# Optimization experiments

Hardware: AMD Instinct MI355X
Metric: run time of the kernel (lower is better)

The kernel has to match this reference:

```python
import jax, jax.numpy as jnp
import numpy as np

N_QUBITS = 8
N_Q_LAYERS = 4
TARGET = 0
B, N, H = 64, 512, 512


def _apply_1q(state, U, w):
    # apply 2x2 complex gate U on wire w of state with shape (2,)*n
    state = jnp.tensordot(U, state, axes=((1,), (w,)))
    return jnp.moveaxis(state, 0, w)


def _cnot(state, c, t):
    s0 = jnp.take(state, 0, axis=c)
    s1 = jnp.take(state, 1, axis=c)
    t_ = t - 1 if t > c else t
    s1 = jnp.flip(s1, axis=t_)  # X on target where control=1
    return jnp.stack([s0, s1], axis=c)


def _ry(theta):
    c, s = jnp.cos(theta / 2), jnp.sin(theta / 2)
    return jnp.stack([jnp.stack([c, -s]), jnp.stack([s, c])]).astype(jnp.complex64)


def _rx(theta):
    c, s = jnp.cos(theta / 2), jnp.sin(theta / 2)
    z = jnp.zeros_like(c)
    re = jnp.stack([jnp.stack([c, z]), jnp.stack([z, c])])
    im = jnp.stack([jnp.stack([z, s]), jnp.stack([s, z])])
    return (re.astype(jnp.complex64) - 1j * im.astype(jnp.complex64))


def _circuit(angles, weights):
    # AngleEmbedding(rotation='Y') + BasicEntanglerLayers(RX + CNOT ring) + <Z_i>
    n = N_QUBITS
    state = jnp.zeros((2,) * n, dtype=jnp.complex64).at[(0,) * n].set(1.0)
    for w in range(n):
        state = _apply_1q(state, _ry(angles[w]), w)
    for l in range(N_Q_LAYERS):
        for w in range(n):
            state = _apply_1q(state, _rx(weights[l, w]), w)
        for w in range(n):
            state = _cnot(state, w, (w + 1) % n)
    probs = state.real ** 2 + state.imag ** 2
    zs = []
    for i in range(n):
        p = probs.sum(axis=tuple(a for a in range(n) if a != i))  # [2]
        zs.append(p[0] - p[1])
    return jnp.stack(zs)  # [n_qubits]


def setup_inputs() -> dict:
    key = jax.random.key(0)
    ks = jax.random.split(key, 10)
    adj = jax.random.uniform(ks[1], (N, N), dtype=jnp.float32)
    norm_adj = adj / adj.sum(axis=1, keepdims=True)  # row-normalized adjacency
    sH = 1.0 / np.sqrt(H)
    return {
        "x": jax.random.normal(ks[0], (B, N, H), dtype=jnp.float32),
        "norm_adj": norm_adj,
        "W_gcn_w": jax.random.normal(ks[2], (H, H), dtype=jnp.float32) * sH,
        "W_gcn_b": jax.random.normal(ks[3], (H,), dtype=jnp.float32) * sH,
        "pre_w": jax.random.normal(ks[4], (N_QUBITS, H), dtype=jnp.float32) * sH,
        "pre_b": jax.random.normal(ks[5], (N_QUBITS,), dtype=jnp.float32) * sH,
        "post_w": jax.random.normal(ks[6], (H, N_QUBITS), dtype=jnp.float32) * (1.0 / np.sqrt(N_QUBITS)),
        "post_b": jax.random.normal(ks[7], (H,), dtype=jnp.float32) * (1.0 / np.sqrt(N_QUBITS)),
        "q_weights": jax.random.uniform(ks[8], (N_Q_LAYERS, N_QUBITS), dtype=jnp.float32) * 2.0 * jnp.pi,
    }


def reference(x, norm_adj, W_gcn_w, W_gcn_b, pre_w, pre_b, post_w, post_b, q_weights):
    # classical GCN aggregation over all N nodes
    x_agg = jnp.einsum('ij,bjh->bih', norm_adj, x)  # [B,N,H]
    x_agg = jax.nn.gelu(x_agg @ W_gcn_w.T + W_gcn_b, approximate=False)
    # dropout is identity in eval mode
    tgt = x_agg[:, TARGET, :]  # [B,H]
    x_qin = jnp.tanh(tgt @ pre_w.T + pre_b) * jnp.pi  # [B,n_qubits]
    q_out = jax.vmap(lambda a: _circuit(a, q_weights))(x_qin)  # [B,n_qubits]
    q_out = q_out @ post_w.T + post_b  # [B,H]
    out = x_agg.at[:, TARGET, :].set(q_out)
    return out
```

## Files before the change

### kernel.cpp

```cpp
#include <hip/hip_runtime.h>
#include <hip/hip_bf16.h>
#include <math.h>

#define B_  64
#define D_  512
#define NQ  8
#define NL  4

typedef __bf16 bf16;
typedef float  f32x4  __attribute__((ext_vector_type(4)));
typedef bf16   bf16x8 __attribute__((ext_vector_type(8)));

__device__ __forceinline__ void async_load16(const bf16* g, bf16* l) {
    __builtin_amdgcn_global_load_lds(
        (const __attribute__((address_space(1))) void*)g,
        (__attribute__((address_space(3))) void*)l, 16, 0, 0);
}

__global__ __launch_bounds__(256) void convert_kernel(const float* __restrict__ src,
                                                      bf16* __restrict__ dst, int n8) {
    int i = blockIdx.x * 256 + threadIdx.x;
    if (i < n8) {
        const float4 v0 = *(const float4*)(src + (size_t)i * 8);
        const float4 v1 = *(const float4*)(src + (size_t)i * 8 + 4);
        bf16x8 p;
        p[0] = (bf16)v0.x; p[1] = (bf16)v0.y; p[2] = (bf16)v0.z; p[3] = (bf16)v0.w;
        p[4] = (bf16)v1.x; p[5] = (bf16)v1.y; p[6] = (bf16)v1.z; p[7] = (bf16)v1.w;
        *(bf16x8*)(dst + (size_t)i * 8) = p;
    }
}

__global__ __launch_bounds__(256) void convert2_kernel(const float* __restrict__ s0,
                                                       const float* __restrict__ s1,
                                                       bf16* __restrict__ dst, int n8each) {
    int i = blockIdx.x * 256 + threadIdx.x;
    if (i < 2 * n8each) {
        const float* s = (i < n8each) ? (s0 + (size_t)i * 8)
                                      : (s1 + (size_t)(i - n8each) * 8);
        const float4 v0 = *(const float4*)s;
        const float4 v1 = *(const float4*)(s + 4);
        bf16x8 p;
        p[0] = (bf16)v0.x; p[1] = (bf16)v0.y; p[2] = (bf16)v0.z; p[3] = (bf16)v0.w;
        p[4] = (bf16)v1.x; p[5] = (bf16)v1.y; p[6] = (bf16)v1.z; p[7] = (bf16)v1.w;
        *(bf16x8*)(dst + (size_t)i * 8) = p;
    }
}

template <int GELU>
__global__ __launch_bounds__(256) void gemm_nt_dma(const bf16* __restrict__ A,
                                                   const bf16* __restrict__ Bv,
                                                   const float* __restrict__ bias,
                                                   void* __restrict__ Cout) {
    __shared__ bf16 As[2][128 * 64];
    __shared__ bf16 Bs[2][128 * 64];

    const int flat = blockIdx.y * 16 + blockIdx.x;
    const int xcd  = flat & 7;
    const int idx  = flat >> 3;
    const int b    = (xcd << 3) | (idx >> 4);
    const int tile = idx & 15;
    const int m0   = (tile >> 2) * 128;
    const int n0   = (tile & 3) * 128;

    const int t    = threadIdx.x;
    const int lane = t & 63;
    const int w    = t >> 6;
    const int wr   = (w >> 1) * 64;
    const int wc   = (w & 1) * 64;
    const int l15  = lane & 15;
    const int quad = lane >> 4;

    f32x4 acc[4][4];
    for (int i = 0; i < 4; i++)
        for (int j = 0; j < 4; j++) acc[i][j] = (f32x4)(0.0f);

    const bf16* Bb = Bv + (size_t)b * D_ * D_;

    const int rl = lane >> 3;
    const int ck = (lane & 7) ^ rl;

    #pragma unroll
    for (int j = 0; j < 4; j++) {
        const int rbase = w * 32 + j * 8;
        async_load16(A  + (size_t)(m0 + rbase + rl) * D_ + ck * 8, &As[0][rbase * 64]);
        async_load16(Bb + (size_t)(n0 + rbase + rl) * D_ + ck * 8, &Bs[0][rbase * 64]);
    }
    __syncthreads();

    #pragma unroll
    for (int s = 0; s < 8; s++) {
        const int p = s & 1;
        if (s < 7) {
            const int k0 = (s + 1) * 64;
            #pragma unroll
            for (int j = 0; j < 4; j++) {
                const int rbase = w * 32 + j * 8;
                async_load16(A  + (size_t)(m0 + rbase + rl) * D_ + k0 + ck * 8,
                             &As[p ^ 1][rbase * 64]);
                async_load16(Bb + (size_t)(n0 + rbase + rl) * D_ + k0 + ck * 8,
                             &Bs[p ^ 1][rbase * 64]);
            }
        }
        #pragma unroll
        for (int kk = 0; kk < 2; kk++) {
            bf16x8 af[4], bfr[4];
            #pragma unroll
            for (int mt = 0; mt < 4; mt++) {
                const int row = wr + mt * 16 + l15;
                const int sl  = (kk * 4 + quad) ^ (l15 & 7);
                af[mt] = *(const bf16x8*)&As[p][row * 64 + sl * 8];
            }
            #pragma unroll
            for (int nt = 0; nt < 4; nt++) {
                const int row = wc + nt * 16 + l15;
                const int sl  = (kk * 4 + quad) ^ (l15 & 7);
                bfr[nt] = *(const bf16x8*)&Bs[p][row * 64 + sl * 8];
            }
            #pragma unroll
            for (int mt = 0; mt < 4; mt++)
                #pragma unroll
                for (int nt = 0; nt < 4; nt++)
                    acc[mt][nt] = __builtin_amdgcn_mfma_f32_16x16x32_bf16(af[mt], bfr[nt], acc[mt][nt], 0, 0, 0);
        }
        __syncthreads();
    }

    if (GELU == 0) {
        bf16* Cb = (bf16*)Cout + (size_t)b * D_ * D_;
        for (int mt = 0; mt < 4; mt++) {
            int row = m0 + wr + mt * 16 + quad * 4;
            for (int nt = 0; nt < 4; nt++) {
                int col = n0 + wc + nt * 16 + l15;
                for (int r = 0; r < 4; r++)
                    Cb[(size_t)(row + r) * D_ + col] = (bf16)acc[mt][nt][r];
            }
        }
    } else {
        float* Cb = (float*)Cout + (size_t)b * D_ * D_;
        for (int mt = 0; mt < 4; mt++) {
            int row = m0 + wr + mt * 16 + quad * 4;
            for (int nt = 0; nt < 4; nt++) {
                int col = n0 + wc + nt * 16 + l15;
                float bv = bias[col];
                for (int r = 0; r < 4; r++) {
                    float v = acc[mt][nt][r] + bv;
                    Cb[(size_t)(row + r) * D_ + col] = 0.5f * v * (1.0f + erff(v * 0.70710678118654752f));
                }
            }
        }
    }
}

#define PITCH 40
template <int GELU>
__global__ __launch_bounds__(256) void gemm_nt_legacy(const float* __restrict__ A,
                                                      const bf16* __restrict__ Bv,
                                                      const float* __restrict__ bias,
                                                      void* __restrict__ Cout) {
    __shared__ bf16 As[128 * PITCH];
    __shared__ bf16 Bs[128 * 32];
    const int b    = blockIdx.y;
    const int tile = blockIdx.x;
    const int m0   = (tile >> 2) * 128;
    const int n0   = (tile & 3) * 128;
    const int t    = threadIdx.x;
    const int lane = t & 63;
    const int w    = t >> 6;
    const int wr   = (w >> 1) * 64;
    const int wc   = (w & 1) * 64;
    const int l15  = lane & 15;
    const int quad = lane >> 4;

    f32x4 acc[4][4];
    for (int i = 0; i < 4; i++)
        for (int j = 0; j < 4; j++) acc[i][j] = (f32x4)(0.0f);

    const bf16* Bb = Bv + (size_t)b * D_ * D_;

    for (int k0 = 0; k0 < D_; k0 += 32) {
        for (int c = t; c < 512; c += 256) {
            int row = c >> 2, ch = c & 3;
            const float* s = A + (size_t)(m0 + row) * D_ + k0 + ch * 8;
            const float4 v0 = *(const float4*)s;
            const float4 v1 = *(const float4*)(s + 4);
            bf16x8 p;
            p[0] = (bf16)v0.x; p[1] = (bf16)v0.y; p[2] = (bf16)v0.z; p[3] = (bf16)v0.w;
            p[4] = (bf16)v1.x; p[5] = (bf16)v1.y; p[6] = (bf16)v1.z; p[7] = (bf16)v1.w;
            *(bf16x8*)&As[row * PITCH + ch * 8] = p;
        }
        {
            int rl = lane >> 2;
            int kchunk = (lane & 3) ^ ((lane >> 3) & 3);
            #pragma unroll
            for (int j = 0; j < 2; j++) {
                int rbase = w * 32 + j * 16;
                async_load16(Bb + (size_t)(n0 + rbase + rl) * D_ + k0 + kchunk * 8, &Bs[rbase * 32]);
            }
        }
        __syncthreads();
        bf16x8 af[4], bfr[4];
        #pragma unroll
        for (int mt = 0; mt < 4; mt++)
            af[mt] = *(const bf16x8*)&As[(wr + mt * 16 + l15) * PITCH + quad * 8];
        #pragma unroll
        for (int nt = 0; nt < 4; nt++) {
            int row = wc + nt * 16 + l15;
            int kx  = quad ^ ((l15 >> 1) & 3);
            bfr[nt] = *(const bf16x8*)&Bs[row * 32 + kx * 8];
        }
        #pragma unroll
        for (int mt = 0; mt < 4; mt++)
            #pragma unroll
            for (int nt = 0; nt < 4; nt++)
                acc[mt][nt] = __builtin_amdgcn_mfma_f32_16x16x32_bf16(af[mt], bfr[nt], acc[mt][nt], 0, 0, 0);
        __syncthreads();
    }

    if (GELU == 0) {
        bf16* Cb = (bf16*)Cout + (size_t)b * D_ * D_;
        for (int mt = 0; mt < 4; mt++) {
            int row = m0 + wr + mt * 16 + quad * 4;
            for (int nt = 0; nt < 4; nt++) {
                int col = n0 + wc + nt * 16 + l15;
                for (int r = 0; r < 4; r++)
                    Cb[(size_t)(row + r) * D_ + col] = (bf16)acc[mt][nt][r];
            }
        }
    } else {
        float* Cb = (float*)Cout + (size_t)b * D_ * D_;
        for (int mt = 0; mt < 4; mt++) {
            int row = m0 + wr + mt * 16 + quad * 4;
            for (int nt = 0; nt < 4; nt++) {
                int col = n0 + wc + nt * 16 + l15;
                float bv = bias[col];
                for (int r = 0; r < 4; r++) {
                    float v = acc[mt][nt][r] + bv;
                    Cb[(size_t)(row + r) * D_ + col] = 0.5f * v * (1.0f + erff(v * 0.70710678118654752f));
                }
            }
        }
    }
}

__global__ __launch_bounds__(64) void quantum_kernel(float* __restrict__ out,
                                                     const float* __restrict__ pre_w,
                                                     const float* __restrict__ pre_b,
                                                     const float* __restrict__ post_w,
                                                     const float* __restrict__ post_b,
                                                     const float* __restrict__ qw) {
    const int b = blockIdx.x;
    const int l = threadIdx.x;
    float* row0 = out + (size_t)b * D_ * D_;

    float tg[8];
    #pragma unroll
    for (int j = 0; j < 8; j++) tg[j] = row0[l + 64 * j];

    float ang[NQ];
    #pragma unroll
    for (int q = 0; q < NQ; q++) {
        float s = 0.f;
        #pragma unroll
        for (int j = 0; j < 8; j++) s += tg[j] * pre_w[q * D_ + l + 64 * j];
        #pragma unroll
        for (int m = 32; m >= 1; m >>= 1) s += __shfl_xor(s, m, 64);
        ang[q] = tanhf(s + pre_b[q]) * 3.14159265358979323846f;
    }

    float cw[NQ], sw[NQ];
    #pragma unroll
    for (int w = 0; w < NQ; w++) { cw[w] = cosf(0.5f * ang[w]); sw[w] = sinf(0.5f * ang[w]); }
    float re[4], im[4];
    #pragma unroll
    for (int r = 0; r < 4; r++) {
        int idx = l * 4 + r;
        float a = 1.f;
        #pragma unroll
        for (int w = 0; w < NQ; w++) a *= ((idx >> (7 - w)) & 1) ? sw[w] : cw[w];
        re[r] = a; im[r] = 0.f;
    }

    for (int lay = 0; lay < NL; lay++) {
        #pragma unroll
        for (int w = 0; w < 6; w++) {
            float th = 0.5f * qw[lay * NQ + w];
            float c = cosf(th), s = sinf(th);
            int m = 1 << (5 - w);
            #pragma unroll
            for (int r = 0; r < 4; r++) {
                float pre_ = __shfl_xor(re[r], m, 64);
                float pim_ = __shfl_xor(im[r], m, 64);
                re[r] = c * re[r] + s * pim_;
                im[r] = c * im[r] - s * pre_;
            }
        }
        {
            float th = 0.5f * qw[lay * NQ + 6];
            float c = cosf(th), s = sinf(th);
            float or0 = re[0], or1 = re[1], or2 = re[2], or3 = re[3];
            float oi0 = im[0], oi1 = im[1], oi2 = im[2], oi3 = im[3];
            re[0] = c * or0 + s * oi2;  im[0] = c * oi0 - s * or2;
            re[1] = c * or1 + s * oi3;  im[1] = c * oi1 - s * or3;
            re[2] = c * or2 + s * oi0;  im[2] = c * oi2 - s * or0;
            re[3] = c * or3 + s * oi1;  im[3] = c * oi3 - s * or1;
        }
        {
            float th = 0.5f * qw[lay * NQ + 7];
            float c = cosf(th), s = sinf(th);
            float or0 = re[0], or1 = re[1], or2 = re[2], or3 = re[3];
            float oi0 = im[0], oi1 = im[1], oi2 = im[2], oi3 = im[3];
            re[0] = c * or0 + s * oi1;  im[0] = c * oi0 - s * or1;
            re[1] = c * or1 + s * oi0;  im[1] = c * oi1 - s * or0;
            re[2] = c * or2 + s * oi3;  im[2] = c * oi2 - s * or3;
            re[3] = c * or3 + s * oi2;  im[3] = c * oi3 - s * or2;
        }
        #pragma unroll
        for (int w = 0; w < 5; w++) {
            int cb = 7 - w, tb = 6 - w;
            int tm = 1 << (tb - 2);
            bool ctl = (l >> (cb - 2)) & 1;
            #pragma unroll
            for (int r = 0; r < 4; r++) {
                float pre_ = __shfl_xor(re[r], tm, 64);
                float pim_ = __shfl_xor(im[r], tm, 64);
                re[r] = ctl ? pre_ : re[r];
                im[r] = ctl ? pim_ : im[r];
            }
        }
        {
            bool ctl = l & 1;
            float t0 = re[0], t1 = re[1], t2 = re[2], t3 = re[3];
            float u0 = im[0], u1 = im[1], u2 = im[2], u3 = im[3];
            re[0] = ctl ? t2 : t0;  re[1] = ctl ? t3 : t1;
            re[2] = ctl ? t0 : t2;  re[3] = ctl ? t1 : t3;
            im[0] = ctl ? u2 : u0;  im[1] = ctl ? u3 : u1;
            im[2] = ctl ? u0 : u2;  im[3] = ctl ? u1 : u3;
        }
        {
            float t2 = re[2], t3 = re[3], u2 = im[2], u3 = im[3];
            re[2] = t3; re[3] = t2; im[2] = u3; im[3] = u2;
        }
        {
            #pragma unroll
            for (int r = 0; r < 4; r++) {
                float pre_ = __shfl_xor(re[r], 32, 64);
                float pim_ = __shfl_xor(im[r], 32, 64);
                if (r & 1) { re[r] = pre_; im[r] = pim_; }
            }
        }
    }

    float pr[4];
    #pragma unroll
    for (int r = 0; r < 4; r++) pr[r] = re[r] * re[r] + im[r] * im[r];
    float z[NQ];
    #pragma unroll
    for (int q = 0; q < NQ; q++) {
        int bit = 7 - q;
        float s = 0.f;
        #pragma unroll
        for (int r = 0; r < 4; r++) {
            int idx = l * 4 + r;
            s += ((idx >> bit) & 1) ? -pr[r] : pr[r];
        }
        #pragma unroll
        for (int m = 32; m >= 1; m >>= 1) s += __shfl_xor(s, m, 64);
        z[q] = s;
    }

    #pragma unroll
    for (int j = 0; j < 8; j++) {
        int h = l + 64 * j;
        float v = post_b[h];
        #pragma unroll
        for (int q = 0; q < NQ; q++) v += z[q] * post_w[h * NQ + q];
        row0[h] = v;
    }
}

extern "C" void kernel_launch(void* const* d_in, const int* in_sizes, int n_in,
                              void* d_out, int out_size, void* d_ws, size_t ws_size,
                              hipStream_t stream) {
    const float* x        = (const float*)d_in[0];
    const float* norm_adj = (const float*)d_in[1];
    const float* W_gcn_w  = (const float*)d_in[2];
    const float* W_gcn_b  = (const float*)d_in[3];
    const float* pre_w    = (const float*)d_in[4];
    const float* pre_b    = (const float*)d_in[5];
    const float* post_w   = (const float*)d_in[6];
    const float* post_b   = (const float*)d_in[7];
    const float* q_w      = (const float*)d_in[8];
    float* out = (float*)d_out;

    bf16* xbf = (bf16*)d_out;
    bf16* Yt  = (bf16*)d_ws;

    const int n8_x = B_ * D_ * D_ / 8;
    const int n8_m = D_ * D_ / 8;
    convert_kernel<<<(n8_x + 255) / 256, 256, 0, stream>>>(x, xbf, n8_x);

    dim3 grid(16, B_);
    const size_t MB32 = (size_t)32 * 1024 * 1024;
    if (ws_size >= MB32 + 2 * 1024 * 1024) {
        bf16* Wbf   = (bf16*)((char*)d_ws + MB32);
        bf16* adjbf = Wbf + D_ * D_;
        convert2_kernel<<<(2 * n8_m + 255) / 256, 256, 0, stream>>>(W_gcn_w, norm_adj, Wbf, n8_m);
        gemm_nt_dma<0><<<grid, 256, 0, stream>>>(Wbf, xbf, nullptr, (void*)Yt);
        gemm_nt_dma<1><<<grid, 256, 0, stream>>>(adjbf, Yt, W_gcn_b, (void*)out);
    } else {
        gemm_nt_legacy<0><<<grid, 256, 0, stream>>>(W_gcn_w, xbf, nullptr, (void*)Yt);
        gemm_nt_legacy<1><<<grid, 256, 0, stream>>>(norm_adj, Yt, W_gcn_b, (void*)out);
    }

    quantum_kernel<<<B_, 64, 0, stream>>>(out, pre_w, pre_b, post_w, post_b, q_w);
}
```

Before: 202.7 us.

## Fuse fp32-to-bf16 conversion of x into the first GEMM's operand load

Result: slower. 217.5 us (+7.3%).

```diff
diff --git a/kernel.cpp b/kernel.cpp
--- a/kernel.cpp
+++ b/kernel.cpp
@@ -43,6 +43,129 @@
         p[0] = (bf16)v0.x; p[1] = (bf16)v0.y; p[2] = (bf16)v0.z; p[3] = (bf16)v0.w;
         p[4] = (bf16)v1.x; p[5] = (bf16)v1.y; p[6] = (bf16)v1.z; p[7] = (bf16)v1.w;
         *(bf16x8*)(dst + (size_t)i * 8) = p;
+    }
+}
+
+__global__ __launch_bounds__(256) void gemm_fused1(const bf16* __restrict__ A,
+                                                   const float* __restrict__ X,
+                                                   void* __restrict__ Cout) {
+    __shared__ bf16 As[2][128 * 64];
+    __shared__ bf16 Bs[2][128 * 64];
+
+    const int flat = blockIdx.y * 16 + blockIdx.x;
+    const int xcd  = flat & 7;
+    const int idx  = flat >> 3;
+    const int b    = (xcd << 3) | (idx >> 4);
+    const int tile = idx & 15;
+    const int m0   = (tile >> 2) * 128;
+    const int n0   = (tile & 3) * 128;
+
+    const int t    = threadIdx.x;
+    const int lane = t & 63;
+    const int w    = t >> 6;
+    const int wr   = (w >> 1) * 64;
+    const int wc   = (w & 1) * 64;
+    const int l15  = lane & 15;
+    const int quad = lane >> 4;
+
+    f32x4 acc[4][4];
+    for (int i = 0; i < 4; i++)
+        for (int j = 0; j < 4; j++) acc[i][j] = (f32x4)(0.0f);
+
+    const float* Xb = X + (size_t)b * D_ * D_;
+
+    const int rl = lane >> 3;
+    const int ck = (lane & 7) ^ rl;
+
+    const int brow = t >> 3;
+    const int bg   = (t & 7) ^ (brow & 7);
+    const float* xbase = Xb + (size_t)(n0 + brow) * D_ + bg * 8;
+
+    float4 breg[8];
+
+    #pragma unroll
+    for (int i = 0; i < 4; i++) {
+        const float* sp = xbase + (size_t)(32 * i) * D_;
+        breg[2 * i]     = *(const float4*)sp;
+        breg[2 * i + 1] = *(const float4*)(sp + 4);
+    }
+    #pragma unroll
+    for (int j = 0; j < 4; j++) {
+        const int rbase = w * 32 + j * 8;
+        async_load16(A + (size_t)(m0 + rbase + rl) * D_ + ck * 8, &As[0][rbase * 64]);
+    }
+    #pragma unroll
+    for (int i = 0; i < 4; i++) {
+        bf16x8 pk;
+        pk[0] = (bf16)breg[2 * i].x;     pk[1] = (bf16)breg[2 * i].y;
+        pk[2] = (bf16)breg[2 * i].z;     pk[3] = (bf16)breg[2 * i].w;
+        pk[4] = (bf16)breg[2 * i + 1].x; pk[5] = (bf16)breg[2 * i + 1].y;
+        pk[6] = (bf16)breg[2 * i + 1].z; pk[7] = (bf16)breg[2 * i + 1].w;
+        *(bf16x8*)&Bs[0][(t + 256 * i) * 8] = pk;
+    }
+    __syncthreads();
+
+    #pragma unroll
+    for (int s = 0; s < 8; s++) {
+        const int p = s & 1;
+        if (s < 7) {
+            const int k0 = (s + 1) * 64;
+            #pragma unroll
+            for (int i = 0; i < 4; i++) {
+                const float* sp = xbase + (size_t)(32 * i) * D_ + k0;
+                breg[2 * i]     = *(const float4*)sp;
+                breg[2 * i + 1] = *(const float4*)(sp + 4);
+            }
+            #pragma unroll
+            for (int j = 0; j < 4; j++) {
+                const int rbase = w * 32 + j * 8;
+                async_load16(A + (size_t)(m0 + rbase + rl) * D_ + k0 + ck * 8,
+                             &As[p ^ 1][rbase * 64]);
+            }
+        }
+        #pragma unroll
+        for (int kk = 0; kk < 2; kk++) {
+            bf16x8 af[4], bfr[4];
+            #pragma unroll
+            for (int mt = 0; mt < 4; mt++) {
+                const int row = wr + mt * 16 + l15;
+                const int sl  = (kk * 4 + quad) ^ (l15 & 7);
+                af[mt] = *(const bf16x8*)&As[p][row * 64 + sl * 8];
+            }
+            #pragma unroll
+            for (int nt = 0; nt < 4; nt++) {
+                const int row = wc + nt * 16 + l15;
+                const int sl  = (kk * 4 + quad) ^ (l15 & 7);
+                bfr[nt] = *(const bf16x8*)&Bs[p][row * 64 + sl * 8];
+            }
+            #pragma unroll
+            for (int mt = 0; mt < 4; mt++)
+                #pragma unroll
+                for (int nt = 0; nt < 4; nt++)
+                    acc[mt][nt] = __builtin_amdgcn_mfma_f32_16x16x32_bf16(af[mt], bfr[nt], acc[mt][nt], 0, 0, 0);
+        }
+        if (s < 7) {
+            #pragma unroll
+            for (int i = 0; i < 4; i++) {
+                bf16x8 pk;
+                pk[0] = (bf16)breg[2 * i].x;     pk[1] = (bf16)breg[2 * i].y;
+                pk[2] = (bf16)breg[2 * i].z;     pk[3] = (bf16)breg[2 * i].w;
+                pk[4] = (bf16)breg[2 * i + 1].x; pk[5] = (bf16)breg[2 * i + 1].y;
+                pk[6] = (bf16)breg[2 * i + 1].z; pk[7] = (bf16)breg[2 * i + 1].w;
+                *(bf16x8*)&Bs[p ^ 1][(t + 256 * i) * 8] = pk;
+            }
+        }
+        __syncthreads();
+    }
+
+    bf16* Cb = (bf16*)Cout + (size_t)b * D_ * D_;
+    for (int mt = 0; mt < 4; mt++) {
+        int row = m0 + wr + mt * 16 + quad * 4;
+        for (int nt = 0; nt < 4; nt++) {
+            int col = n0 + wc + nt * 16 + l15;
+            for (int r = 0; r < 4; r++)
+                Cb[(size_t)(row + r) * D_ + col] = (bf16)acc[mt][nt][r];
+        }
     }
 }
 
@@ -392,22 +515,21 @@
     const float* q_w      = (const float*)d_in[8];
     float* out = (float*)d_out;
 
-    bf16* xbf = (bf16*)d_out;
-    bf16* Yt  = (bf16*)d_ws;
-
-    const int n8_x = B_ * D_ * D_ / 8;
+    bf16* Yt = (bf16*)d_ws;
+
     const int n8_m = D_ * D_ / 8;
-    convert_kernel<<<(n8_x + 255) / 256, 256, 0, stream>>>(x, xbf, n8_x);
-
     dim3 grid(16, B_);
     const size_t MB32 = (size_t)32 * 1024 * 1024;
     if (ws_size >= MB32 + 2 * 1024 * 1024) {
         bf16* Wbf   = (bf16*)((char*)d_ws + MB32);
         bf16* adjbf = Wbf + D_ * D_;
         convert2_kernel<<<(2 * n8_m + 255) / 256, 256, 0, stream>>>(W_gcn_w, norm_adj, Wbf, n8_m);
-        gemm_nt_dma<0><<<grid, 256, 0, stream>>>(Wbf, xbf, nullptr, (void*)Yt);
+        gemm_fused1<<<grid, 256, 0, stream>>>(Wbf, x, (void*)Yt);
         gemm_nt_dma<1><<<grid, 256, 0, stream>>>(adjbf, Yt, W_gcn_b, (void*)out);
     } else {
+        bf16* xbf = (bf16*)d_out;
+        const int n8_x = B_ * D_ * D_ / 8;
+        convert_kernel<<<(n8_x + 255) / 256, 256, 0, stream>>>(x, xbf, n8_x);
         gemm_nt_legacy<0><<<grid, 256, 0, stream>>>(W_gcn_w, xbf, nullptr, (void*)Yt);
         gemm_nt_legacy<1><<<grid, 256, 0, stream>>>(norm_adj, Yt, W_gcn_b, (void*)out);
     }
```

## Enlarge GEMM tiles to 256x256 with 512 threads and fuse input conversions

Applied to the files above, without the earlier changes.

Result: slower. 273.6 us (+35.0%).

```diff
diff --git a/kernel.cpp b/kernel.cpp
--- a/kernel.cpp
+++ b/kernel.cpp
@@ -15,6 +15,38 @@
     __builtin_amdgcn_global_load_lds(
         (const __attribute__((address_space(1))) void*)g,
         (__attribute__((address_space(3))) void*)l, 16, 0, 0);
+}
+
+__global__ __launch_bounds__(256) void convert_all(const float* __restrict__ x,
+                                                   const float* __restrict__ w,
+                                                   const float* __restrict__ adj,
+                                                   bf16* __restrict__ xbf,
+                                                   bf16* __restrict__ wbf,
+                                                   bf16* __restrict__ adjbf,
+                                                   int n8x, int n8m) {
+    int i = blockIdx.x * 256 + threadIdx.x;
+    const float* s;
+    bf16* d;
+    if (i < n8x) {
+        s = x + (size_t)i * 8;
+        d = xbf + (size_t)i * 8;
+    } else if (i < n8x + n8m) {
+        int j = i - n8x;
+        s = w + (size_t)j * 8;
+        d = wbf + (size_t)j * 8;
+    } else if (i < n8x + 2 * n8m) {
+        int j = i - n8x - n8m;
+        s = adj + (size_t)j * 8;
+        d = adjbf + (size_t)j * 8;
+    } else {
+        return;
+    }
+    const float4 v0 = *(const float4*)s;
+    const float4 v1 = *(const float4*)(s + 4);
+    bf16x8 p;
+    p[0] = (bf16)v0.x; p[1] = (bf16)v0.y; p[2] = (bf16)v0.z; p[3] = (bf16)v0.w;
+    p[4] = (bf16)v1.x; p[5] = (bf16)v1.y; p[6] = (bf16)v1.z; p[7] = (bf16)v1.w;
+    *(bf16x8*)d = p;
 }
 
 __global__ __launch_bounds__(256) void convert_kernel(const float* __restrict__ src,
@@ -30,48 +62,34 @@
     }
 }
 
-__global__ __launch_bounds__(256) void convert2_kernel(const float* __restrict__ s0,
-                                                       const float* __restrict__ s1,
-                                                       bf16* __restrict__ dst, int n8each) {
-    int i = blockIdx.x * 256 + threadIdx.x;
-    if (i < 2 * n8each) {
-        const float* s = (i < n8each) ? (s0 + (size_t)i * 8)
-                                      : (s1 + (size_t)(i - n8each) * 8);
-        const float4 v0 = *(const float4*)s;
-        const float4 v1 = *(const float4*)(s + 4);
-        bf16x8 p;
-        p[0] = (bf16)v0.x; p[1] = (bf16)v0.y; p[2] = (bf16)v0.z; p[3] = (bf16)v0.w;
-        p[4] = (bf16)v1.x; p[5] = (bf16)v1.y; p[6] = (bf16)v1.z; p[7] = (bf16)v1.w;
-        *(bf16x8*)(dst + (size_t)i * 8) = p;
-    }
-}
-
 template <int GELU>
-__global__ __launch_bounds__(256) void gemm_nt_dma(const bf16* __restrict__ A,
+__global__ __launch_bounds__(512) void gemm_nt_256(const bf16* __restrict__ A,
                                                    const bf16* __restrict__ Bv,
                                                    const float* __restrict__ bias,
                                                    void* __restrict__ Cout) {
-    __shared__ bf16 As[2][128 * 64];
-    __shared__ bf16 Bs[2][128 * 64];
-
-    const int flat = blockIdx.y * 16 + blockIdx.x;
+    __shared__ bf16 As[2][256 * 64];
+    __shared__ bf16 Bs[2][256 * 64];
+
+    const int flat = blockIdx.y * 4 + blockIdx.x;
     const int xcd  = flat & 7;
     const int idx  = flat >> 3;
-    const int b    = (xcd << 3) | (idx >> 4);
-    const int tile = idx & 15;
-    const int m0   = (tile >> 2) * 128;
-    const int n0   = (tile & 3) * 128;
+    const int b    = (xcd << 3) | (idx >> 2);
+    const int tile = idx & 3;
+    const int m0   = (tile >> 1) * 256;
+    const int n0   = (tile & 1) * 256;
 
     const int t    = threadIdx.x;
     const int lane = t & 63;
     const int w    = t >> 6;
-    const int wr   = (w >> 1) * 64;
-    const int wc   = (w & 1) * 64;
+    const int wr   = (w >> 2) * 128;
+    const int wc   = (w & 3) * 64;
     const int l15  = lane & 15;
     const int quad = lane >> 4;
 
-    f32x4 acc[4][4];
-    for (int i = 0; i < 4; i++)
+    f32x4 acc[8][4];
+    #pragma unroll
+    for (int i = 0; i < 8; i++)
+        #pragma unroll
         for (int j = 0; j < 4; j++) acc[i][j] = (f32x4)(0.0f);
 
     const bf16* Bb = Bv + (size_t)b * D_ * D_;
@@ -103,9 +121,9 @@
         }
         #pragma unroll
         for (int kk = 0; kk < 2; kk++) {
-            bf16x8 af[4], bfr[4];
-            #pragma unroll
-            for (int mt = 0; mt < 4; mt++) {
+            bf16x8 af[8], bfr[4];
+            #pragma unroll
+            for (int mt = 0; mt < 8; mt++) {
                 const int row = wr + mt * 16 + l15;
                 const int sl  = (kk * 4 + quad) ^ (l15 & 7);
                 af[mt] = *(const bf16x8*)&As[p][row * 64 + sl * 8];
@@ -117,7 +135,7 @@
                 bfr[nt] = *(const bf16x8*)&Bs[p][row * 64 + sl * 8];
             }
             #pragma unroll
-            for (int mt = 0; mt < 4; mt++)
+            for (int mt = 0; mt < 8; mt++)
                 #pragma unroll
                 for (int nt = 0; nt < 4; nt++)
                     acc[mt][nt] = __builtin_amdgcn_mfma_f32_16x16x32_bf16(af[mt], bfr[nt], acc[mt][nt], 0, 0, 0);
@@ -127,7 +145,7 @@
 
     if (GELU == 0) {
         bf16* Cb = (bf16*)Cout + (size_t)b * D_ * D_;
-        for (int mt = 0; mt < 4; mt++) {
+        for (int mt = 0; mt < 8; mt++) {
             int row = m0 + wr + mt * 16 + quad * 4;
             for (int nt = 0; nt < 4; nt++) {
                 int col = n0 + wc + nt * 16 + l15;
@@ -137,7 +155,7 @@
         }
     } else {
         float* Cb = (float*)Cout + (size_t)b * D_ * D_;
-        for (int mt = 0; mt < 4; mt++) {
+        for (int mt = 0; mt < 8; mt++) {
             int row = m0 + wr + mt * 16 + quad * 4;
             for (int nt = 0; nt < 4; nt++) {
                 int col = n0 + wc + nt * 16 + l15;
@@ -397,17 +415,19 @@
 
     const int n8_x = B_ * D_ * D_ / 8;
     const int n8_m = D_ * D_ / 8;
-    convert_kernel<<<(n8_x + 255) / 256, 256, 0, stream>>>(x, xbf, n8_x);
-
-    dim3 grid(16, B_);
+
     const size_t MB32 = (size_t)32 * 1024 * 1024;
     if (ws_size >= MB32 + 2 * 1024 * 1024) {
         bf16* Wbf   = (bf16*)((char*)d_ws + MB32);
         bf16* adjbf = Wbf + D_ * D_;
-        convert2_kernel<<<(2 * n8_m + 255) / 256, 256, 0, stream>>>(W_gcn_w, norm_adj, Wbf, n8_m);
-        gemm_nt_dma<0><<<grid, 256, 0, stream>>>(Wbf, xbf, nullptr, (void*)Yt);
-        gemm_nt_dma<1><<<grid, 256, 0, stream>>>(adjbf, Yt, W_gcn_b, (void*)out);
+        convert_all<<<(n8_x + 2 * n8_m + 255) / 256, 256, 0, stream>>>(
+            x, W_gcn_w, norm_adj, xbf, Wbf, adjbf, n8_x, n8_m);
+        dim3 grid(4, B_);
+        gemm_nt_256<0><<<grid, 512, 0, stream>>>(Wbf, xbf, nullptr, (void*)Yt);
+        gemm_nt_256<1><<<grid, 512, 0, stream>>>(adjbf, Yt, W_gcn_b, (void*)out);
     } else {
+        dim3 grid(16, B_);
+        convert_kernel<<<(n8_x + 255) / 256, 256, 0, stream>>>(x, xbf, n8_x);
         gemm_nt_legacy<0><<<grid, 256, 0, stream>>>(W_gcn_w, xbf, nullptr, (void*)Yt);
         gemm_nt_legacy<1><<<grid, 256, 0, stream>>>(norm_adj, Yt, W_gcn_b, (void*)out);
     }
```

## Fuse convert, both GEMMs and quantum stage into one cooperative persistent kernel

Applied to the files above, without the earlier changes.

New measurement: 700.1 us. 245% more time.

```diff
diff --git a/kernel.cpp b/kernel.cpp
--- a/kernel.cpp
+++ b/kernel.cpp
@@ -1,6 +1,9 @@
 #include <hip/hip_runtime.h>
+#include <hip/hip_cooperative_groups.h>
 #include <hip/hip_bf16.h>
 #include <math.h>
+
+namespace cg = cooperative_groups;
 
 #define B_  64
 #define D_  512
@@ -17,52 +20,30 @@
         (__attribute__((address_space(3))) void*)l, 16, 0, 0);
 }
 
-__global__ __launch_bounds__(256) void convert_kernel(const float* __restrict__ src,
-                                                      bf16* __restrict__ dst, int n8) {
-    int i = blockIdx.x * 256 + threadIdx.x;
-    if (i < n8) {
-        const float4 v0 = *(const float4*)(src + (size_t)i * 8);
-        const float4 v1 = *(const float4*)(src + (size_t)i * 8 + 4);
-        bf16x8 p;
-        p[0] = (bf16)v0.x; p[1] = (bf16)v0.y; p[2] = (bf16)v0.z; p[3] = (bf16)v0.w;
-        p[4] = (bf16)v1.x; p[5] = (bf16)v1.y; p[6] = (bf16)v1.z; p[7] = (bf16)v1.w;
-        *(bf16x8*)(dst + (size_t)i * 8) = p;
-    }
-}
-
-__global__ __launch_bounds__(256) void convert2_kernel(const float* __restrict__ s0,
-                                                       const float* __restrict__ s1,
-                                                       bf16* __restrict__ dst, int n8each) {
-    int i = blockIdx.x * 256 + threadIdx.x;
-    if (i < 2 * n8each) {
-        const float* s = (i < n8each) ? (s0 + (size_t)i * 8)
-                                      : (s1 + (size_t)(i - n8each) * 8);
-        const float4 v0 = *(const float4*)s;
-        const float4 v1 = *(const float4*)(s + 4);
-        bf16x8 p;
-        p[0] = (bf16)v0.x; p[1] = (bf16)v0.y; p[2] = (bf16)v0.z; p[3] = (bf16)v0.w;
-        p[4] = (bf16)v1.x; p[5] = (bf16)v1.y; p[6] = (bf16)v1.z; p[7] = (bf16)v1.w;
-        *(bf16x8*)(dst + (size_t)i * 8) = p;
-    }
+__device__ __forceinline__ void conv8(const float* __restrict__ s, bf16* __restrict__ d) {
+    const float4 v0 = *(const float4*)s;
+    const float4 v1 = *(const float4*)(s + 4);
+    bf16x8 p;
+    p[0] = (bf16)v0.x; p[1] = (bf16)v0.y; p[2] = (bf16)v0.z; p[3] = (bf16)v0.w;
+    p[4] = (bf16)v1.x; p[5] = (bf16)v1.y; p[6] = (bf16)v1.z; p[7] = (bf16)v1.w;
+    *(bf16x8*)d = p;
 }
 
 template <int GELU>
-__global__ __launch_bounds__(256) void gemm_nt_dma(const bf16* __restrict__ A,
-                                                   const bf16* __restrict__ Bv,
-                                                   const float* __restrict__ bias,
-                                                   void* __restrict__ Cout) {
-    __shared__ bf16 As[2][128 * 64];
-    __shared__ bf16 Bs[2][128 * 64];
-
-    const int flat = blockIdx.y * 16 + blockIdx.x;
-    const int xcd  = flat & 7;
-    const int idx  = flat >> 3;
+__device__ __forceinline__ void gemm128_tile(const bf16* __restrict__ A,
+                                             const bf16* __restrict__ Bv,
+                                             const float* __restrict__ bias,
+                                             void* __restrict__ Cout,
+                                             int v, int t,
+                                             bf16* __restrict__ As,
+                                             bf16* __restrict__ Bs) {
+    const int xcd  = v & 7;
+    const int idx  = v >> 3;
     const int b    = (xcd << 3) | (idx >> 4);
     const int tile = idx & 15;
     const int m0   = (tile >> 2) * 128;
     const int n0   = (tile & 3) * 128;
 
-    const int t    = threadIdx.x;
     const int lane = t & 63;
     const int w    = t >> 6;
     const int wr   = (w >> 1) * 64;
@@ -71,7 +52,9 @@
     const int quad = lane >> 4;
 
     f32x4 acc[4][4];
+    #pragma unroll
     for (int i = 0; i < 4; i++)
+        #pragma unroll
         for (int j = 0; j < 4; j++) acc[i][j] = (f32x4)(0.0f);
 
     const bf16* Bb = Bv + (size_t)b * D_ * D_;
@@ -82,23 +65,25 @@
     #pragma unroll
     for (int j = 0; j < 4; j++) {
         const int rbase = w * 32 + j * 8;
-        async_load16(A  + (size_t)(m0 + rbase + rl) * D_ + ck * 8, &As[0][rbase * 64]);
-        async_load16(Bb + (size_t)(n0 + rbase + rl) * D_ + ck * 8, &Bs[0][rbase * 64]);
+        async_load16(A  + (size_t)(m0 + rbase + rl) * D_ + ck * 8, As + rbase * 64);
+        async_load16(Bb + (size_t)(n0 + rbase + rl) * D_ + ck * 8, Bs + rbase * 64);
     }
     __syncthreads();
 
-    #pragma unroll
+    #pragma unroll 1
     for (int s = 0; s < 8; s++) {
         const int p = s & 1;
+        const bf16* Asp = As + p * (128 * 64);
+        const bf16* Bsp = Bs + p * (128 * 64);
         if (s < 7) {
             const int k0 = (s + 1) * 64;
+            bf16* Asn = As + (p ^ 1) * (128 * 64);
+            bf16* Bsn = Bs + (p ^ 1) * (128 * 64);
             #pragma unroll
             for (int j = 0; j < 4; j++) {
                 const int rbase = w * 32 + j * 8;
-                async_load16(A  + (size_t)(m0 + rbase + rl) * D_ + k0 + ck * 8,
-                             &As[p ^ 1][rbase * 64]);
-                async_load16(Bb + (size_t)(n0 + rbase + rl) * D_ + k0 + ck * 8,
-                             &Bs[p ^ 1][rbase * 64]);
+                async_load16(A  + (size_t)(m0 + rbase + rl) * D_ + k0 + ck * 8, Asn + rbase * 64);
+                async_load16(Bb + (size_t)(n0 + rbase + rl) * D_ + k0 + ck * 8, Bsn + rbase * 64);
             }
         }
         #pragma unroll
@@ -108,13 +93,13 @@
             for (int mt = 0; mt < 4; mt++) {
                 const int row = wr + mt * 16 + l15;
                 const int sl  = (kk * 4 + quad) ^ (l15 & 7);
-                af[mt] = *(const bf16x8*)&As[p][row * 64 + sl * 8];
+                af[mt] = *(const bf16x8*)&Asp[row * 64 + sl * 8];
             }
             #pragma unroll
             for (int nt = 0; nt < 4; nt++) {
                 const int row = wc + nt * 16 + l15;
                 const int sl  = (kk * 4 + quad) ^ (l15 & 7);
-                bfr[nt] = *(const bf16x8*)&Bs[p][row * 64 + sl * 8];
+                bfr[nt] = *(const bf16x8*)&Bsp[row * 64 + sl * 8];
             }
             #pragma unroll
             for (int mt = 0; mt < 4; mt++)
@@ -127,28 +112,261 @@
 
     if (GELU == 0) {
         bf16* Cb = (bf16*)Cout + (size_t)b * D_ * D_;
+        #pragma unroll
         for (int mt = 0; mt < 4; mt++) {
             int row = m0 + wr + mt * 16 + quad * 4;
+            #pragma unroll
             for (int nt = 0; nt < 4; nt++) {
                 int col = n0 + wc + nt * 16 + l15;
+                #pragma unroll
                 for (int r = 0; r < 4; r++)
                     Cb[(size_t)(row + r) * D_ + col] = (bf16)acc[mt][nt][r];
             }
         }
     } else {
         float* Cb = (float*)Cout + (size_t)b * D_ * D_;
+        #pragma unroll
         for (int mt = 0; mt < 4; mt++) {
             int row = m0 + wr + mt * 16 + quad * 4;
+            #pragma unroll
             for (int nt = 0; nt < 4; nt++) {
                 int col = n0 + wc + nt * 16 + l15;
                 float bv = bias[col];
+                #pragma unroll
                 for (int r = 0; r < 4; r++) {
-                    float v = acc[mt][nt][r] + bv;
-                    Cb[(size_t)(row + r) * D_ + col] = 0.5f * v * (1.0f + erff(v * 0.70710678118654752f));
+                    float v2 = acc[mt][nt][r] + bv;
+                    Cb[(size_t)(row + r) * D_ + col] = 0.5f * v2 * (1.0f + erff(v2 * 0.70710678118654752f));
                 }
             }
         }
     }
+}
+
+__device__ void quantum_body(float* __restrict__ out,
+                             const float* __restrict__ pre_w,
+                             const float* __restrict__ pre_b,
+                             const float* __restrict__ post_w,
+                             const float* __restrict__ post_b,
+                             const float* __restrict__ qw,
+                             int b, int l) {
+    float* row0 = out + (size_t)b * D_ * D_;
+
+    float tg[8];
+    #pragma unroll
+    for (int j = 0; j < 8; j++) tg[j] = row0[l + 64 * j];
+
+    float ang[NQ];
+    #pragma unroll
+    for (int q = 0; q < NQ; q++) {
+        float s = 0.f;
+        #pragma unroll
+        for (int j = 0; j < 8; j++) s += tg[j] * pre_w[q * D_ + l + 64 * j];
+        #pragma unroll
+        for (int m = 32; m >= 1; m >>= 1) s += __shfl_xor(s, m, 64);
+        ang[q] = tanhf(s + pre_b[q]) * 3.14159265358979323846f;
+    }
+
+    float cw[NQ], sw[NQ];
+    #pragma unroll
+    for (int w = 0; w < NQ; w++) { cw[w] = cosf(0.5f * ang[w]); sw[w] = sinf(0.5f * ang[w]); }
+    float re[4], im[4];
+    #pragma unroll
+    for (int r = 0; r < 4; r++) {
+        int idx = l * 4 + r;
+        float a = 1.f;
+        #pragma unroll
+        for (int w = 0; w < NQ; w++) a *= ((idx >> (7 - w)) & 1) ? sw[w] : cw[w];
+        re[r] = a; im[r] = 0.f;
+    }
+
+    for (int lay = 0; lay < NL; lay++) {
+        #pragma unroll
+        for (int w = 0; w < 6; w++) {
+            float th = 0.5f * qw[lay * NQ + w];
+            float c = cosf(th), s = sinf(th);
+            int m = 1 << (5 - w);
+            #pragma unroll
+            for (int r = 0; r < 4; r++) {
+                float pre_ = __shfl_xor(re[r], m, 64);
+                float pim_ = __shfl_xor(im[r], m, 64);
+                re[r] = c * re[r] + s * pim_;
+                im[r] = c * im[r] - s * pre_;
+            }
+        }
+        {
+            float th = 0.5f * qw[lay * NQ + 6];
+            float c = cosf(th), s = sinf(th);
+            float or0 = re[0], or1 = re[1], or2 = re[2], or3 = re[3];
+            float oi0 = im[0], oi1 = im[1], oi2 = im[2], oi3 = im[3];
+            re[0] = c * or0 + s * oi2;  im[0] = c * oi0 - s * or2;
+            re[1] = c * or1 + s * oi3;  im[1] = c * oi1 - s * or3;
+            re[2] = c * or2 + s * oi0;  im[2] = c * oi2 - s * or0;
+            re[3] = c * or3 + s * oi1;  im[3] = c * oi3 - s * or1;
+        }
+        {
+            float th = 0.5f * qw[lay * NQ + 7];
+            float c = cosf(th), s = sinf(th);
+            float or0 = re[0], or1 = re[1], or2 = re[2], or3 = re[3];
+            float oi0 = im[0], oi1 = im[1], oi2 = im[2], oi3 = im[3];
+            re[0] = c * or0 + s * oi1;  im[0] = c * oi0 - s * or1;
+            re[1] = c * or1 + s * oi0;  im[1] = c * oi1 - s * or0;
+            re[2] = c * or2 + s * oi3;  im[2] = c * oi2 - s * or3;
+            re[3] = c * or3 + s * oi2;  im[3] = c * oi3 - s * or2;
+        }
+        #pragma unroll
+        for (int w = 0; w < 5; w++) {
+            int cb = 7 - w, tb = 6 - w;
+            int tm = 1 << (tb - 2);
+            bool ctl = (l >> (cb - 2)) & 1;
+            #pragma unroll
+            for (int r = 0; r < 4; r++) {
+                float pre_ = __shfl_xor(re[r], tm, 64);
+                float pim_ = __shfl_xor(im[r], tm, 64);
+                re[r] = ctl ? pre_ : re[r];
+                im[r] = ctl ? pim_ : im[r];
+            }
+        }
+        {
+            bool ctl = l & 1;
+            float t0 = re[0], t1 = re[1], t2 = re[2], t3 = re[3];
+            float u0 = im[0], u1 = im[1], u2 = im[2], u3 = im[3];
+            re[0] = ctl ? t2 : t0;  re[1] = ctl ? t3 : t1;
+            re[2] = ctl ? t0 : t2;  re[3] = ctl ? t1 : t3;
+            im[0] = ctl ? u2 : u0;  im[1] = ctl ? u3 : u1;
+            im[2] = ctl ? u0 : u2;  im[3] = ctl ? u1 : u3;
+        }
+        {
+            float t2 = re[2], t3 = re[3], u2 = im[2], u3 = im[3];
+            re[2] = t3; re[3] = t2; im[2] = u3; im[3] = u2;
+        }
+        {
+            #pragma unroll
+            for (int r = 0; r < 4; r++) {
+                float pre_ = __shfl_xor(re[r], 32, 64);
+                float pim_ = __shfl_xor(im[r], 32, 64);
+                if (r & 1) { re[r] = pre_; im[r] = pim_; }
+            }
+        }
+    }
+
+    float pr[4];
+    #pragma unroll
+    for (int r = 0; r < 4; r++) pr[r] = re[r] * re[r] + im[r] * im[r];
+    float z[NQ];
+    #pragma unroll
+    for (int q = 0; q < NQ; q++) {
+        int bit = 7 - q;
+        float s = 0.f;
+        #pragma unroll
+        for (int r = 0; r < 4; r++) {
+            int idx = l * 4 + r;
+            s += ((idx >> bit) & 1) ? -pr[r] : pr[r];
+        }
+        #pragma unroll
+        for (int m = 32; m >= 1; m >>= 1) s += __shfl_xor(s, m, 64);
+        z[q] = s;
+    }
+
+    #pragma unroll
+    for (int j = 0; j < 8; j++) {
+        int h = l + 64 * j;
+        float v = post_b[h];
+        #pragma unroll
+        for (int q = 0; q < NQ; q++) v += z[q] * post_w[h * NQ + q];
+        row0[h] = v;
+    }
+}
+
+__global__ __launch_bounds__(256, 2) void mega(const float* __restrict__ x,
+                                               const float* __restrict__ W,
+                                               const float* __restrict__ adj,
+                                               const float* __restrict__ bias,
+                                               const float* __restrict__ pre_w,
+                                               const float* __restrict__ pre_b,
+                                               const float* __restrict__ post_w,
+                                               const float* __restrict__ post_b,
+                                               const float* __restrict__ qw,
+                                               bf16* __restrict__ xbf,
+                                               bf16* __restrict__ Wbf,
+                                               bf16* __restrict__ adjbf,
+                                               bf16* __restrict__ Yt,
+                                               float* __restrict__ out) {
+    cg::grid_group grid = cg::this_grid();
+    __shared__ bf16 As[2 * 128 * 64];
+    __shared__ bf16 Bs[2 * 128 * 64];
+
+    const int blk = blockIdx.x;
+    const int t   = threadIdx.x;
+
+    {
+        const int n8x = B_ * D_ * D_ / 8;
+        const int n8m = D_ * D_ / 8;
+        const int total = n8x + 2 * n8m;
+        for (int i = blk * 256 + t; i < total; i += 512 * 256) {
+            if (i < n8x)            conv8(x   + (size_t)i * 8,              xbf   + (size_t)i * 8);
+            else if (i < n8x + n8m) conv8(W   + (size_t)(i - n8x) * 8,      Wbf   + (size_t)(i - n8x) * 8);
+            else                    conv8(adj + (size_t)(i - n8x - n8m) * 8, adjbf + (size_t)(i - n8x - n8m) * 8);
+        }
+    }
+    __threadfence();
+    grid.sync();
+    __threadfence();
+
+    gemm128_tile<0>(Wbf, xbf, nullptr, (void*)Yt, blk,       t, As, Bs);
+    gemm128_tile<0>(Wbf, xbf, nullptr, (void*)Yt, blk + 512, t, As, Bs);
+    __threadfence();
+    grid.sync();
+    __threadfence();
+
+    gemm128_tile<1>(adjbf, Yt, bias, (void*)out, blk,       t, As, Bs);
+    gemm128_tile<1>(adjbf, Yt, bias, (void*)out, blk + 512, t, As, Bs);
+    __threadfence();
+    grid.sync();
+    __threadfence();
+
+    if (blk < 64 && t < 64)
+        quantum_body(out, pre_w, pre_b, post_w, post_b, qw, blk, t);
+}
+
+__global__ __launch_bounds__(256) void convert_all_k(const float* __restrict__ x,
+                                                     const float* __restrict__ w,
+                                                     const float* __restrict__ adj,
+                                                     bf16* __restrict__ xbf,
+                                                     bf16* __restrict__ wbf,
+                                                     bf16* __restrict__ adjbf,
+                                                     int n8x, int n8m) {
+    const int total = n8x + 2 * n8m;
+    for (int i = blockIdx.x * 256 + threadIdx.x; i < total; i += gridDim.x * 256) {
+        if (i < n8x)            conv8(x   + (size_t)i * 8,               xbf   + (size_t)i * 8);
+        else if (i < n8x + n8m) conv8(w   + (size_t)(i - n8x) * 8,       wbf   + (size_t)(i - n8x) * 8);
+        else                    conv8(adj + (size_t)(i - n8x - n8m) * 8,  adjbf + (size_t)(i - n8x - n8m) * 8);
+    }
+}
+
+template <int GELU>
+__global__ __launch_bounds__(256) void gemm128_k(const bf16* __restrict__ A,
+                                                 const bf16* __restrict__ Bv,
+                                                 const float* __restrict__ bias,
+                                                 void* __restrict__ Cout) {
+    __shared__ bf16 As[2 * 128 * 64];
+    __shared__ bf16 Bs[2 * 128 * 64];
+    const int v = blockIdx.y * 16 + blockIdx.x;
+    gemm128_tile<GELU>(A, Bv, bias, Cout, v, threadIdx.x, As, Bs);
+}
+
+__global__ __launch_bounds__(64) void quantum_k(float* __restrict__ out,
+                                                const float* __restrict__ pre_w,
+                                                const float* __restrict__ pre_b,
+                                                const float* __restrict__ post_w,
+                                                const float* __restrict__ post_b,
+                                                const float* __restrict__ qw) {
+    quantum_body(out, pre_w, pre_b, post_w, post_b, qw, blockIdx.x, threadIdx.x);
+}
+
+__global__ __launch_bounds__(256) void convert_kernel(const float* __restrict__ src,
+                                                      bf16* __restrict__ dst, int n8) {
+    int i = blockIdx.x * 256 + threadIdx.x;
+    if (i < n8) conv8(src + (size_t)i * 8, dst + (size_t)i * 8);
 }
 
 #define PITCH 40
@@ -172,7 +390,9 @@
     const int quad = lane >> 4;
 
     f32x4 acc[4][4];
+    #pragma unroll
     for (int i = 0; i < 4; i++)
+        #pragma unroll
         for (int j = 0; j < 4; j++) acc[i][j] = (f32x4)(0.0f);
 
     const bf16* Bb = Bv + (size_t)b * D_ * D_;
@@ -218,163 +438,33 @@
 
     if (GELU == 0) {
         bf16* Cb = (bf16*)Cout + (size_t)b * D_ * D_;
+        #pragma unroll
         for (int mt = 0; mt < 4; mt++) {
             int row = m0 + wr + mt * 16 + quad * 4;
+            #pragma unroll
             for (int nt = 0; nt < 4; nt++) {
                 int col = n0 + wc + nt * 16 + l15;
+                #pragma unroll
                 for (int r = 0; r < 4; r++)
                     Cb[(size_t)(row + r) * D_ + col] = (bf16)acc[mt][nt][r];
             }
         }
     } else {
         float* Cb = (float*)Cout + (size_t)b * D_ * D_;
+        #pragma unroll
         for (int mt = 0; mt < 4; mt++) {
             int row = m0 + wr + mt * 16 + quad * 4;
+            #pragma unroll
             for (int nt = 0; nt < 4; nt++) {
                 int col = n0 + wc + nt * 16 + l15;
                 float bv = bias[col];
+                #pragma unroll
                 for (int r = 0; r < 4; r++) {
                     float v = acc[mt][nt][r] + bv;
                     Cb[(size_t)(row + r) * D_ + col] = 0.5f * v * (1.0f + erff(v * 0.70710678118654752f));
                 }
             }
         }
-    }
-}
-
-__global__ __launch_bounds__(64) void quantum_kernel(float* __restrict__ out,
-                                                     const float* __restrict__ pre_w,
-                                                     const float* __restrict__ pre_b,
-                                                     const float* __restrict__ post_w,
-                                                     const float* __restrict__ post_b,
-                                                     const float* __restrict__ qw) {
-    const int b = blockIdx.x;
-    const int l = threadIdx.x;
-    float* row0 = out + (size_t)b * D_ * D_;
-
-    float tg[8];
-    #pragma unroll
-    for (int j = 0; j < 8; j++) tg[j] = row0[l + 64 * j];
-
-    float ang[NQ];
-    #pragma unroll
-    for (int q = 0; q < NQ; q++) {
-        float s = 0.f;
-        #pragma unroll
-        for (int j = 0; j < 8; j++) s += tg[j] * pre_w[q * D_ + l + 64 * j];
-        #pragma unroll
-        for (int m = 32; m >= 1; m >>= 1) s += __shfl_xor(s, m, 64);
-        ang[q] = tanhf(s + pre_b[q]) * 3.14159265358979323846f;
-    }
-
-    float cw[NQ], sw[NQ];
-    #pragma unroll
-    for (int w = 0; w < NQ; w++) { cw[w] = cosf(0.5f * ang[w]); sw[w] = sinf(0.5f * ang[w]); }
-    float re[4], im[4];
-    #pragma unroll
-    for (int r = 0; r < 4; r++) {
-        int idx = l * 4 + r;
-        float a = 1.f;
-        #pragma unroll
-        for (int w = 0; w < NQ; w++) a *= ((idx >> (7 - w)) & 1) ? sw[w] : cw[w];
-        re[r] = a; im[r] = 0.f;
-    }
-
-    for (int lay = 0; lay < NL; lay++) {
-        #pragma unroll
-        for (int w = 0; w < 6; w++) {
-            float th = 0.5f * qw[lay * NQ + w];
-            float c = cosf(th), s = sinf(th);
-            int m = 1 << (5 - w);
-            #pragma unroll
-            for (int r = 0; r < 4; r++) {
-                float pre_ = __shfl_xor(re[r], m, 64);
-                float pim_ = __shfl_xor(im[r], m, 64);
-                re[r] = c * re[r] + s * pim_;
-                im[r] = c * im[r] - s * pre_;
-            }
-        }
-        {
-            float th = 0.5f * qw[lay * NQ + 6];
-            float c = cosf(th), s = sinf(th);
-            float or0 = re[0], or1 = re[1], or2 = re[2], or3 = re[3];
-            float oi0 = im[0], oi1 = im[1], oi2 = im[2], oi3 = im[3];
-            re[0] = c * or0 + s * oi2;  im[0] = c * oi0 - s * or2;
-            re[1] = c * or1 + s * oi3;  im[1] = c * oi1 - s * or3;
-            re[2] = c * or2 + s * oi0;  im[2] = c * oi2 - s * or0;
-            re[3] = c * or3 + s * oi1;  im[3] = c * oi3 - s * or1;
-        }
-        {
-            float th = 0.5f * qw[lay * NQ + 7];
-            float c = cosf(th), s = sinf(th);
-            float or0 = re[0], or1 = re[1], or2 = re[2], or3 = re[3];
-            float oi0 = im[0], oi1 = im[1], oi2 = im[2], oi3 = im[3];
-            re[0] = c * or0 + s * oi1;  im[0] = c * oi0 - s * or1;
-            re[1] = c * or1 + s * oi0;  im[1] = c * oi1 - s * or0;
-            re[2] = c * or2 + s * oi3;  im[2] = c * oi2 - s * or3;
-            re[3] = c * or3 + s * oi2;  im[3] = c * oi3 - s * or2;
-        }
-        #pragma unroll
-        for (int w = 0; w < 5; w++) {
-            int cb = 7 - w, tb = 6 - w;
-            int tm = 1 << (tb - 2);
-            bool ctl = (l >> (cb - 2)) & 1;
-            #pragma unroll
-            for (int r = 0; r < 4; r++) {
-                float pre_ = __shfl_xor(re[r], tm, 64);
-                float pim_ = __shfl_xor(im[r], tm, 64);
-                re[r] = ctl ? pre_ : re[r];
-                im[r] = ctl ? pim_ : im[r];
-            }
-        }
-        {
-            bool ctl = l & 1;
-            float t0 = re[0], t1 = re[1], t2 = re[2], t3 = re[3];
-            float u0 = im[0], u1 = im[1], u2 = im[2], u3 = im[3];
-            re[0] = ctl ? t2 : t0;  re[1] = ctl ? t3 : t1;
-            re[2] = ctl ? t0 : t2;  re[3] = ctl ? t1 : t3;
-            im[0] = ctl ? u2 : u0;  im[1] = ctl ? u3 : u1;
-            im[2] = ctl ? u0 : u2;  im[3] = ctl ? u1 : u3;
-        }
-        {
-            float t2 = re[2], t3 = re[3], u2 = im[2], u3 = im[3];
-            re[2] = t3; re[3] = t2; im[2] = u3; im[3] = u2;
-        }
-        {
-            #pragma unroll
-            for (int r = 0; r < 4; r++) {
-                float pre_ = __shfl_xor(re[r], 32, 64);
-                float pim_ = __shfl_xor(im[r], 32, 64);
-                if (r & 1) { re[r] = pre_; im[r] = pim_; }
-            }
-        }
-    }
-
-    float pr[4];
-    #pragma unroll
-    for (int r = 0; r < 4; r++) pr[r] = re[r] * re[r] + im[r] * im[r];
-    float z[NQ];
-    #pragma unroll
-    for (int q = 0; q < NQ; q++) {
-        int bit = 7 - q;
-        float s = 0.f;
-        #pragma unroll
-        for (int r = 0; r < 4; r++) {
-            int idx = l * 4 + r;
-            s += ((idx >> bit) & 1) ? -pr[r] : pr[r];
-        }
-        #pragma unroll
-        for (int m = 32; m >= 1; m >>= 1) s += __shfl_xor(s, m, 64);
-        z[q] = s;
-    }
-
-    #pragma unroll
-    for (int j = 0; j < 8; j++) {
-        int h = l + 64 * j;
-        float v = post_b[h];
-        #pragma unroll
-        for (int q = 0; q < NQ; q++) v += z[q] * post_w[h * NQ + q];
-        row0[h] = v;
     }
 }
 
@@ -397,20 +487,34 @@
 
     const int n8_x = B_ * D_ * D_ / 8;
     const int n8_m = D_ * D_ / 8;
-    convert_kernel<<<(n8_x + 255) / 256, 256, 0, stream>>>(x, xbf, n8_x);
-
-    dim3 grid(16, B_);
+
     const size_t MB32 = (size_t)32 * 1024 * 1024;
     if (ws_size >= MB32 + 2 * 1024 * 1024) {
         bf16* Wbf   = (bf16*)((char*)d_ws + MB32);
         bf16* adjbf = Wbf + D_ * D_;
-        convert2_kernel<<<(2 * n8_m + 255) / 256, 256, 0, stream>>>(W_gcn_w, norm_adj, Wbf, n8_m);
-        gemm_nt_dma<0><<<grid, 256, 0, stream>>>(Wbf, xbf, nullptr, (void*)Yt);
-        gemm_nt_dma<1><<<grid, 256, 0, stream>>>(adjbf, Yt, W_gcn_b, (void*)out);
+
+        void* args[] = {
+            (void*)&x, (void*)&W_gcn_w, (void*)&norm_adj, (void*)&W_gcn_b,
+            (void*)&pre_w, (void*)&pre_b, (void*)&post_w, (void*)&post_b,
+            (void*)&q_w, (void*)&xbf, (void*)&Wbf, (void*)&adjbf,
+            (void*)&Yt, (void*)&out
+        };
+        hipError_t e = hipLaunchCooperativeKernel((const void*)mega,
+                                                  dim3(512), dim3(256),
+                                                  args, 0, stream);
+        if (e != hipSuccess) {
+            convert_all_k<<<2048, 256, 0, stream>>>(x, W_gcn_w, norm_adj,
+                                                    xbf, Wbf, adjbf, n8_x, n8_m);
+            dim3 grid(16, B_);
+            gemm128_k<0><<<grid, 256, 0, stream>>>(Wbf, xbf, nullptr, (void*)Yt);
+            gemm128_k<1><<<grid, 256, 0, stream>>>(adjbf, Yt, W_gcn_b, (void*)out);
+            quantum_k<<<B_, 64, 0, stream>>>(out, pre_w, pre_b, post_w, post_b, q_w);
+        }
     } else {
+        dim3 grid(16, B_);
+        convert_kernel<<<(n8_x + 255) / 256, 256, 0, stream>>>(x, xbf, n8_x);
         gemm_nt_legacy<0><<<grid, 256, 0, stream>>>(W_gcn_w, xbf, nullptr, (void*)Yt);
         gemm_nt_legacy<1><<<grid, 256, 0, stream>>>(norm_adj, Yt, W_gcn_b, (void*)out);
-    }
-
-    quantum_kernel<<<B_, 64, 0, stream>>>(out, pre_w, pre_b, post_w, post_b, q_w);
-}
+        quantum_k<<<B_, 64, 0, stream>>>(out, pre_w, pre_b, post_w, post_b, q_w);
+    }
+}
```
